# Optimization experiments

Hardware: AMD Instinct MI355X
Metric: run time of the kernel (lower is better)

The kernel has to match this reference:

```python
import jax, jax.numpy as jnp
import numpy as np

B, N, D, H, E = 4, 1024, 1024, 2048, 8

def setup_inputs() -> dict:
    key = jax.random.key(0)
    ks = jax.random.split(key, 5)
    return {
        "x": jax.random.normal(ks[0], (B, N, D), dtype=jnp.float32),
        "gate_w": jax.random.normal(ks[1], (D, E), dtype=jnp.float32) * 0.02,
        "gate_b": jnp.zeros((E,), dtype=jnp.float32),
        "w1": jax.random.normal(ks[2], (E, D, H), dtype=jnp.float32) * 0.02,
        "b1": jnp.zeros((E, H), dtype=jnp.float32),
        "w2": jax.random.normal(ks[3], (E, H, D), dtype=jnp.float32) * 0.02,
        "b2": jnp.zeros((E, D), dtype=jnp.float32),
        "gamma": jnp.ones((D,), dtype=jnp.float32),
    }

def reference(x, gate_w, gate_b, w1, b1, w2, b2, gamma):
    b, n, d = x.shape
    e = w1.shape[0]
    xf = x.reshape(b * n, d)                                    # [T, D]
    # gate: softmax over experts, then top-1
    probs = jax.nn.softmax(xf @ gate_w + gate_b, axis=-1)       # [T, E]
    top_val = jnp.max(probs, axis=-1, keepdims=True)            # [T, 1]
    top_idx = jnp.argmax(probs, axis=-1)                        # [T]
    # all-expert FFN (dense reference for masked dispatch; dropout in eval)
    h = jax.nn.gelu(jnp.einsum('td,edh->eth', xf, w1) + b1[:, None, :],
                    approximate=False)                          # [E, T, H]
    eo = jnp.einsum('eth,ehd->etd', h, w2) + b2[:, None, :]     # [E, T, D]
    onehot = jax.nn.one_hot(top_idx, e, dtype=xf.dtype)         # [T, E]
    out = jnp.einsum('etd,te->td', eo, onehot)                  # select routed expert
    y = (xf + out * top_val).reshape(b, n, d)
    # RMSNorm: F.normalize (L2, eps=1e-12) * gamma * sqrt(dim)
    nrm = jnp.linalg.norm(y, axis=-1, keepdims=True)
    y = y / jnp.maximum(nrm, 1e-12) * gamma * np.float32(np.sqrt(d))
    # load-balancing loss (unbiased variance like torch.var)
    importance = probs.sum(axis=0)                              # [E]
    load_loss = jnp.var(importance, ddof=1) / (jnp.mean(importance) ** 2 + 1e-10)
    return jax.nn.gelu(y, approximate=False), load_loss
```

## Files before the change

kernel.cpp:

```cpp
#include <hip/hip_runtime.h>
#include <math.h>

#define T_TOK 4096
#define DIM   1024
#define HID   2048
#define NE    8
#define TMM   128
#define BK    64
#define GATE_BLOCKS (T_TOK / 4)

typedef unsigned int  u32;
typedef unsigned short u16;
typedef __attribute__((ext_vector_type(8))) short bf16x8;
typedef __attribute__((ext_vector_type(4))) float f32x4;

__device__ __forceinline__ float gelu_exact(float v) {
    return 0.5f * v * (1.0f + erff(v * 0.70710678118654752440f));
}

__device__ __forceinline__ float gelu_fast(float x) {
    float u = 1.5957691216057308f * (x + 0.044715f * x * x * x);
    float e = __expf(u);
    float t = 1.f - 2.f / (e + 1.f);
    return 0.5f * x * (1.f + t);
}

__device__ __forceinline__ u16 f2bf(float v) {
    u32 u = __float_as_uint(v);
    u32 r = (u + 0x7FFFu + ((u >> 16) & 1u)) >> 16;
    return (u16)r;
}

__device__ __forceinline__ void gld_lds16(const void* g, void* l) {
    __builtin_amdgcn_global_load_lds(
        (const __attribute__((address_space(1))) u32*)g,
        (__attribute__((address_space(3))) u32*)l,
        16, 0, 0);
}

__device__ __forceinline__ void transpose_body(
    const float* __restrict__ in, u16* __restrict__ out, int R, int C,
    int bx, int by, int bz, float (*tile)[65])
{
    const float* src = in  + (size_t)bz * R * C;
    u16*         dst = out + (size_t)bz * R * C;
    const int c0 = bx * 64, r0 = by * 64;
    const int th = threadIdx.x;

    const int tr  = th >> 4;
    const int tc4 = (th & 15) * 4;
    #pragma unroll
    for (int i = 0; i < 4; i++) {
        const int r = tr + i * 16;
        float4 v = *(const float4*)&src[(size_t)(r0 + r) * C + c0 + tc4];
        tile[r][tc4 + 0] = v.x; tile[r][tc4 + 1] = v.y;
        tile[r][tc4 + 2] = v.z; tile[r][tc4 + 3] = v.w;
    }
    __syncthreads();
    const int cc  = th >> 4;
    const int rr4 = (th & 15) * 4;
    #pragma unroll
    for (int i = 0; i < 4; i++) {
        const int c = cc + i * 16;
        ushort4 o;
        o.x = f2bf(tile[rr4 + 0][c]);
        o.y = f2bf(tile[rr4 + 1][c]);
        o.z = f2bf(tile[rr4 + 2][c]);
        o.w = f2bf(tile[rr4 + 3][c]);
        *(ushort4*)&dst[(size_t)(c0 + c) * R + r0 + rr4] = o;
    }
}

__global__ __launch_bounds__(256) void prep_kernel(
    const float* __restrict__ w1, const float* __restrict__ w2,
    u16* __restrict__ w1t, u16* __restrict__ w2t,
    const float* __restrict__ x, const float* __restrict__ gw,
    const float* __restrict__ gb, float* __restrict__ top_val,
    int* __restrict__ top_idx, float* __restrict__ partial_imp,
    int* __restrict__ partial_cnt)
{
    __shared__ float tile[64][65];
    __shared__ float s_imp[NE];
    __shared__ int   s_cnt[NE];

    const int id = blockIdx.x;
    if (id < 4096) {
        transpose_body(w1, w1t, DIM, HID, id & 31, (id >> 5) & 15, id >> 9, tile);
        return;
    }
    if (id < 8192) {
        const int i2 = id - 4096;
        transpose_body(w2, w2t, HID, DIM, i2 & 15, (i2 >> 4) & 31, i2 >> 9, tile);
        return;
    }

    const int g = id - 8192;
    if (threadIdx.x < NE) { s_imp[threadIdx.x] = 0.f; s_cnt[threadIdx.x] = 0; }
    __syncthreads();

    const int wave = threadIdx.x >> 6;
    const int lane = threadIdx.x & 63;
    const int t = g * 4 + wave;

    float acc[NE];
    #pragma unroll
    for (int e = 0; e < NE; e++) acc[e] = 0.f;

    const float* xr = x + (size_t)t * DIM;
    #pragma unroll 4
    for (int k = lane; k < DIM; k += 64) {
        float xv = xr[k];
        const float* gp = gw + (size_t)k * NE;
        float4 g0 = *(const float4*)gp;
        float4 g1 = *(const float4*)(gp + 4);
        acc[0] += xv * g0.x; acc[1] += xv * g0.y;
        acc[2] += xv * g0.z; acc[3] += xv * g0.w;
        acc[4] += xv * g1.x; acc[5] += xv * g1.y;
        acc[6] += xv * g1.z; acc[7] += xv * g1.w;
    }
    #pragma unroll
    for (int e = 0; e < NE; e++) {
        #pragma unroll
        for (int off = 32; off > 0; off >>= 1)
            acc[e] += __shfl_down(acc[e], off, 64);
    }
    if (lane == 0) {
        float l[NE];
        float m = -1e30f;
        #pragma unroll
        for (int e = 0; e < NE; e++) { l[e] = acc[e] + gb[e]; m = fmaxf(m, l[e]); }
        float s = 0.f;
        #pragma unroll
        for (int e = 0; e < NE; e++) { l[e] = expf(l[e] - m); s += l[e]; }
        float inv = 1.f / s;
        int bi = 0; float bv = -1.f;
        #pragma unroll
        for (int e = 0; e < NE; e++) {
            float p = l[e] * inv;
            atomicAdd(&s_imp[e], p);
            if (p > bv) { bv = p; bi = e; }
        }
        top_val[t] = bv;
        top_idx[t] = bi;
        atomicAdd(&s_cnt[bi], 1);
    }
    __syncthreads();
    if (threadIdx.x < NE) {
        partial_imp[g * NE + threadIdx.x] = s_imp[threadIdx.x];
        partial_cnt[g * NE + threadIdx.x] = s_cnt[threadIdx.x];
    }
}

__global__ __launch_bounds__(256) void plan_kernel(
    const float* __restrict__ partial_imp, const int* __restrict__ partial_cnt,
    int* __restrict__ counts, int* __restrict__ offsets,
    int* __restrict__ tile_e, int* __restrict__ tile_s,
    int* __restrict__ tile_rows, int* __restrict__ ntiles,
    float* __restrict__ loss_out)
{
    __shared__ float rimp[32][NE];
    __shared__ int   rcnt[32][NE];
    const int th = threadIdx.x;
    const int e = th & 7, chunk = th >> 3;
    float si = 0.f; int sc = 0;
    #pragma unroll 8
    for (int i = 0; i < GATE_BLOCKS / 32; i++) {
        const int b = chunk * (GATE_BLOCKS / 32) + i;
        si += partial_imp[b * NE + e];
        sc += partial_cnt[b * NE + e];
    }
    rimp[chunk][e] = si;
    rcnt[chunk][e] = sc;
    __syncthreads();
    if (th < NE) {
        float s = 0.f; int c = 0;
        for (int i = 0; i < 32; i++) { s += rimp[i][th]; c += rcnt[i][th]; }
        counts[th] = c;
        rimp[0][th] = s;
        rcnt[0][th] = c;
    }
    __syncthreads();
    if (th == 0) {
        int off = 0, nt = 0;
        for (int ee = 0; ee < NE; ee++) {
            offsets[ee] = off;
            const int c = rcnt[0][ee];
            for (int s = 0; s < c; s += TMM) {
                tile_e[nt] = ee;
                tile_s[nt] = off + s;
                tile_rows[nt] = min(TMM, c - s);
                nt++;
            }
            off += c;
        }
        offsets[NE] = off;
        *ntiles = nt;

        float mean = 0.f;
        for (int ee = 0; ee < NE; ee++) mean += rimp[0][ee];
        mean *= (1.0f / NE);
        float var = 0.f;
        for (int ee = 0; ee < NE; ee++) { float d = rimp[0][ee] - mean; var += d * d; }
        var *= (1.0f / (NE - 1));
        loss_out[0] = var / (mean * mean + 1e-10f);
    }
}

__global__ __launch_bounds__(256) void scatter_kernel(
    const int* __restrict__ top_idx, const int* __restrict__ offsets,
    int* __restrict__ cursors, int* __restrict__ sorted_tok)
{
    __shared__ int lcnt[NE], lbase[NE];
    if (threadIdx.x < NE) lcnt[threadIdx.x] = 0;
    __syncthreads();
    const int t = blockIdx.x * blockDim.x + threadIdx.x;
    const int e = top_idx[t];
    const int lrank = atomicAdd(&lcnt[e], 1);
    __syncthreads();
    if (threadIdx.x < NE)
        lbase[threadIdx.x] = atomicAdd(&cursors[threadIdx.x], lcnt[threadIdx.x]);
    __syncthreads();
    sorted_tok[offsets[e] + lbase[e] + lrank] = t;
}

__global__ __launch_bounds__(256) void gather_x_kernel(
    const float* __restrict__ x, const int* __restrict__ sorted_tok,
    u16* __restrict__ xs)
{
    const int s = blockIdx.x;
    const int tok = sorted_tok[s];
    const float* src = x + (size_t)tok * DIM;
    u16* dst = xs + (size_t)s * DIM;
    const int i = threadIdx.x * 4;
    float4 v = *(const float4*)&src[i];
    ushort4 o;
    o.x = f2bf(v.x); o.y = f2bf(v.y); o.z = f2bf(v.z); o.w = f2bf(v.w);
    *(ushort4*)&dst[i] = o;
}

__global__ __launch_bounds__(512, 4) void ffn1_mfma(
    const u16* __restrict__ xs, const u16* __restrict__ w1t,
    const float* __restrict__ b1,
    const int* __restrict__ tile_e, const int* __restrict__ tile_s,
    const int* __restrict__ tile_rows, const int* __restrict__ ntiles,
    u16* __restrict__ h_buf)
{
    const int tile = blockIdx.y;
    if (tile >= *ntiles) return;
    const int e     = tile_e[tile];
    const int sbase = tile_s[tile];
    const int rows  = tile_rows[tile];
    const int nbase = blockIdx.x * 256;

    __shared__ __align__(16) u16 As[128 * BK];
    __shared__ __align__(16) u16 Bs[256 * BK];

    const int th = threadIdx.x;
    const int w  = th >> 6;
    const int l  = th & 63;
    const int wm = w >> 2, wn = w & 3;
    const int lr = l >> 3;
    const int lcs = ((l & 7) ^ lr) * 8;

    const u16* aptr[2];
    #pragma unroll
    for (int c = 0; c < 2; c++) {
        int srow = sbase + c * 64 + w * 8 + lr;
        if (srow > T_TOK - 1) srow = T_TOK - 1;
        aptr[c] = xs + (size_t)srow * DIM + lcs;
    }
    const u16* wb = w1t + (size_t)e * HID * DIM + (size_t)nbase * DIM;
    const u16* bptr[4];
    #pragma unroll
    for (int c = 0; c < 4; c++)
        bptr[c] = wb + (size_t)(c * 64 + w * 8 + lr) * DIM + lcs;

    f32x4 acc[4][4] = {};

    for (int k0 = 0; k0 < DIM; k0 += BK) {
        __syncthreads();
        #pragma unroll
        for (int c = 0; c < 2; c++)
            gld_lds16(aptr[c] + k0, &As[(c * 64 + w * 8) * BK]);
        #pragma unroll
        for (int c = 0; c < 4; c++)
            gld_lds16(bptr[c] + k0, &Bs[(c * 64 + w * 8) * BK]);
        __syncthreads();
        #pragma unroll
        for (int ks = 0; ks < 2; ks++) {
            const int ko = ((ks * 4 + (l >> 4)) ^ (l & 7)) * 8;
            bf16x8 af[4], bfr[4];
            #pragma unroll
            for (int i = 0; i < 4; i++)
                af[i]  = *(const bf16x8*)&As[(wm * 64 + i * 16 + (l & 15)) * BK + ko];
            #pragma unroll
            for (int i = 0; i < 4; i++)
                bfr[i] = *(const bf16x8*)&Bs[(wn * 64 + i * 16 + (l & 15)) * BK + ko];
            #pragma unroll
            for (int mi = 0; mi < 4; mi++)
                #pragma unroll
                for (int ni = 0; ni < 4; ni++)
                    acc[mi][ni] = __builtin_amdgcn_mfma_f32_16x16x32_bf16(
                        af[mi], bfr[ni], acc[mi][ni], 0, 0, 0);
        }
    }

    const int col = l & 15, quad = l >> 4;
    #pragma unroll
    for (int ni = 0; ni < 4; ni++) {
        const int n = nbase + wn * 64 + ni * 16 + col;
        const float bias = b1[e * HID + n];
        #pragma unroll
        for (int mi = 0; mi < 4; mi++) {
            #pragma unroll
            for (int r = 0; r < 4; r++) {
                const int m = wm * 64 + mi * 16 + quad * 4 + r;
                if (m < rows) {
                    float v = acc[mi][ni][r] + bias;
                    h_buf[(size_t)(sbase + m) * HID + n] = f2bf(gelu_fast(v));
                }
            }
        }
    }
}

__global__ __launch_bounds__(256) void ffn2_mfma(
    const u16* __restrict__ h_buf, const u16* __restrict__ w2t,
    const float* __restrict__ b2, const float* __restrict__ x,
    const int* __restrict__ sorted_tok, const float* __restrict__ top_val,
    const int* __restrict__ tile_e, const int* __restrict__ tile_s,
    const int* __restrict__ tile_rows, const int* __restrict__ ntiles,
    float* __restrict__ yout)
{
    const int tile = blockIdx.y;
    if (tile >= *ntiles) return;
    const int e     = tile_e[tile];
    const int sbase = tile_s[tile];
    const int rows  = tile_rows[tile];
    const int nbase = blockIdx.x * 128;

    __shared__ __align__(16) u16 As[128 * BK];
    __shared__ __align__(16) u16 Bs[128 * BK];

    const int th = threadIdx.x;
    const int w  = th >> 6;
    const int l  = th & 63;
    const int wm = w >> 1, wn = w & 1;
    const int lr = l >> 3;
    const int lcs = ((l & 7) ^ lr) * 8;

    const u16* aptr[4];
    #pragma unroll
    for (int c = 0; c < 4; c++) {
        int srow = sbase + w * 32 + c * 8 + lr;
        if (srow > T_TOK - 1) srow = T_TOK - 1;
        aptr[c] = h_buf + (size_t)srow * HID + lcs;
    }
    const u16* wb = w2t + (size_t)e * DIM * HID + (size_t)nbase * HID;
    const u16* bptr[4];
    #pragma unroll
    for (int c = 0; c < 4; c++)
        bptr[c] = wb + (size_t)(w * 32 + c * 8 + lr) * HID + lcs;

    f32x4 acc[4][4] = {};

    for (int k0 = 0; k0 < HID; k0 += BK) {
        __syncthreads();
        #pragma unroll
        for (int c = 0; c < 4; c++)
            gld_lds16(aptr[c] + k0, &As[(w * 32 + c * 8) * BK]);
        #pragma unroll
        for (int c = 0; c < 4; c++)
            gld_lds16(bptr[c] + k0, &Bs[(w * 32 + c * 8) * BK]);
        __syncthreads();
        #pragma unroll
        for (int ks = 0; ks < 2; ks++) {
            const int ko = ((ks * 4 + (l >> 4)) ^ (l & 7)) * 8;
            bf16x8 af[4], bfr[4];
            #pragma unroll
            for (int i = 0; i < 4; i++)
                af[i]  = *(const bf16x8*)&As[(wm * 64 + i * 16 + (l & 15)) * BK + ko];
            #pragma unroll
            for (int i = 0; i < 4; i++)
                bfr[i] = *(const bf16x8*)&Bs[(wn * 64 + i * 16 + (l & 15)) * BK + ko];
            #pragma unroll
            for (int mi = 0; mi < 4; mi++)
                #pragma unroll
                for (int ni = 0; ni < 4; ni++)
                    acc[mi][ni] = __builtin_amdgcn_mfma_f32_16x16x32_bf16(
                        af[mi], bfr[ni], acc[mi][ni], 0, 0, 0);
        }
    }

    const int col = l & 15, quad = l >> 4;
    float bias[4];
    #pragma unroll
    for (int ni = 0; ni < 4; ni++)
        bias[ni] = b2[e * DIM + nbase + wn * 64 + ni * 16 + col];

    #pragma unroll
    for (int mi = 0; mi < 4; mi++) {
        #pragma unroll
        for (int r = 0; r < 4; r++) {
            const int m = wm * 64 + mi * 16 + quad * 4 + r;
            if (m < rows) {
                const int t = sorted_tok[sbase + m];
                const float tv = top_val[t];
                #pragma unroll
                for (int ni = 0; ni < 4; ni++) {
                    const int n = nbase + wn * 64 + ni * 16 + col;
                    float v = acc[mi][ni][r] + bias[ni];
                    yout[(size_t)t * DIM + n] = x[(size_t)t * DIM + n] + v * tv;
                }
            }
        }
    }
}

__global__ __launch_bounds__(256) void norm_kernel(float* __restrict__ y,
                                                   const float* __restrict__ gamma)
{
    const int t = blockIdx.x;
    float* row = y + (size_t)t * DIM;
    const int th = threadIdx.x;
    float4 v = *(const float4*)&row[th * 4];
    float ss = v.x * v.x + v.y * v.y + v.z * v.z + v.w * v.w;

    const int lane = th & 63, wave = th >> 6;
    #pragma unroll
    for (int off = 32; off > 0; off >>= 1) ss += __shfl_down(ss, off, 64);
    __shared__ float red[4];
    if (lane == 0) red[wave] = ss;
    __syncthreads();
    float total = red[0] + red[1] + red[2] + red[3];

    float nrm = sqrtf(total);
    float scale = 32.0f / fmaxf(nrm, 1e-12f);

    float4 g = *(const float4*)&gamma[th * 4];
    float4 o;
    o.x = gelu_exact(v.x * scale * g.x);
    o.y = gelu_exact(v.y * scale * g.y);
    o.z = gelu_exact(v.z * scale * g.z);
    o.w = gelu_exact(v.w * scale * g.w);
    *(float4*)&row[th * 4] = o;
}

extern "C" void kernel_launch(void* const* d_in, const int* in_sizes, int n_in,
                              void* d_out, int out_size, void* d_ws, size_t ws_size,
                              hipStream_t stream) {
    const float* x      = (const float*)d_in[0];
    const float* gate_w = (const float*)d_in[1];
    const float* gate_b = (const float*)d_in[2];
    const float* w1     = (const float*)d_in[3];
    const float* b1     = (const float*)d_in[4];
    const float* w2     = (const float*)d_in[5];
    const float* b2     = (const float*)d_in[6];
    const float* gamma  = (const float*)d_in[7];

    float* out  = (float*)d_out;
    float* loss = out + (size_t)T_TOK * DIM;

    char* ws = (char*)d_ws;
    float* top_val     = (float*)(ws + 0);
    int*   top_idx     = (int*)  (ws + 16384);
    int*   sorted_tok  = (int*)  (ws + 32768);
    int*   counts      = (int*)  (ws + 49152);
    int*   cursors     = (int*)  (ws + 49216);
    int*   offsets     = (int*)  (ws + 49280);
    int*   tile_e      = (int*)  (ws + 49664);
    int*   tile_s      = (int*)  (ws + 50176);
    int*   tile_rows   = (int*)  (ws + 50688);
    int*   ntiles      = (int*)  (ws + 51200);
    float* partial_imp = (float*)(ws + 65536);
    int*   partial_cnt = (int*)  (ws + 98304);
    u16*   x_sorted    = (u16*)  (ws + 131072);
    u16*   h_buf       = (u16*)  (ws + 131072 + 8388608);
    u16*   w1t         = (u16*)  (ws + 131072 + 8388608 + 16777216);
    u16*   w2t         = (u16*)  (ws + 131072 + 8388608 + 16777216 + 33554432);

    hipMemsetAsync(ws + 49216, 0, 64, stream);

    prep_kernel<<<8192 + GATE_BLOCKS, 256, 0, stream>>>(
        w1, w2, w1t, w2t, x, gate_w, gate_b, top_val, top_idx,
        partial_imp, partial_cnt);
    plan_kernel<<<1, 256, 0, stream>>>(partial_imp, partial_cnt, counts,
                                       offsets, tile_e, tile_s, tile_rows,
                                       ntiles, loss);
    scatter_kernel<<<T_TOK / 256, 256, 0, stream>>>(top_idx, offsets, cursors,
                                                    sorted_tok);
    gather_x_kernel<<<T_TOK, 256, 0, stream>>>(x, sorted_tok, x_sorted);

    ffn1_mfma<<<dim3(HID / 256, 40), 512, 0, stream>>>(
        x_sorted, w1t, b1, tile_e, tile_s, tile_rows, ntiles, h_buf);
    ffn2_mfma<<<dim3(DIM / 128, 40), 256, 0, stream>>>(
        h_buf, w2t, b2, x, sorted_tok, top_val, tile_e, tile_s, tile_rows,
        ntiles, out);
    norm_kernel<<<T_TOK, 256, 0, stream>>>(out, gamma);
}
```

Before: 300.3 us.

## Merge plan and scatter kernels, shrink FFN1 tiles, swap grid axes

Widens the transpose stores in the weight-prep kernel to 8-element bf16 vectors. Folds the scatter step into the single-block plan kernel, which removes one launch, the memset and the global atomics on cursors. Shrinks the FFN1 block tile from 128x256 with 512 threads to 128x128 with 256 threads. Swaps grid axes in both FFN kernels so token tiles vary fastest along blockIdx.x. The serial single-block scatter and the smaller FFN1 tiles, which reload the activation tile more often, may offset the gains.

```diff
diff --git a/kernel.cpp b/kernel.cpp
--- a/kernel.cpp
+++ b/kernel.cpp
@@ -12,6 +12,7 @@
 typedef unsigned int  u32;
 typedef unsigned short u16;
 typedef __attribute__((ext_vector_type(8))) short bf16x8;
+typedef __attribute__((ext_vector_type(8))) unsigned short u16x8;
 typedef __attribute__((ext_vector_type(4))) float f32x4;
 
 __device__ __forceinline__ float gelu_exact(float v) {
@@ -57,17 +58,15 @@
         tile[r][tc4 + 2] = v.z; tile[r][tc4 + 3] = v.w;
     }
     __syncthreads();
-    const int cc  = th >> 4;
-    const int rr4 = (th & 15) * 4;
-    #pragma unroll
-    for (int i = 0; i < 4; i++) {
-        const int c = cc + i * 16;
-        ushort4 o;
-        o.x = f2bf(tile[rr4 + 0][c]);
-        o.y = f2bf(tile[rr4 + 1][c]);
-        o.z = f2bf(tile[rr4 + 2][c]);
-        o.w = f2bf(tile[rr4 + 3][c]);
-        *(ushort4*)&dst[(size_t)(c0 + c) * R + r0 + rr4] = o;
+    const int cc  = th >> 3;
+    const int rr8 = (th & 7) * 8;
+    #pragma unroll
+    for (int i = 0; i < 2; i++) {
+        const int c = cc + i * 32;
+        u16x8 o;
+        #pragma unroll
+        for (int j = 0; j < 8; j++) o[j] = f2bf(tile[rr8 + j][c]);
+        *(u16x8*)&dst[(size_t)(c0 + c) * R + r0 + rr8] = o;
     }
 }
 
@@ -151,15 +150,18 @@
     }
 }
 
-__global__ __launch_bounds__(256) void plan_kernel(
+__global__ __launch_bounds__(256) void route_kernel(
     const float* __restrict__ partial_imp, const int* __restrict__ partial_cnt,
-    int* __restrict__ counts, int* __restrict__ offsets,
+    const int* __restrict__ top_idx,
+    int* __restrict__ sorted_tok,
     int* __restrict__ tile_e, int* __restrict__ tile_s,
     int* __restrict__ tile_rows, int* __restrict__ ntiles,
     float* __restrict__ loss_out)
 {
     __shared__ float rimp[32][NE];
     __shared__ int   rcnt[32][NE];
+    __shared__ int   s_off[NE];
+    __shared__ int   s_cur[NE];
     const int th = threadIdx.x;
     const int e = th & 7, chunk = th >> 3;
     float si = 0.f; int sc = 0;
@@ -175,15 +177,15 @@
     if (th < NE) {
         float s = 0.f; int c = 0;
         for (int i = 0; i < 32; i++) { s += rimp[i][th]; c += rcnt[i][th]; }
-        counts[th] = c;
         rimp[0][th] = s;
         rcnt[0][th] = c;
+        s_cur[th] = 0;
     }
     __syncthreads();
     if (th == 0) {
         int off = 0, nt = 0;
         for (int ee = 0; ee < NE; ee++) {
-            offsets[ee] = off;
+            s_off[ee] = off;
             const int c = rcnt[0][ee];
             for (int s = 0; s < c; s += TMM) {
                 tile_e[nt] = ee;
@@ -193,7 +195,6 @@
             }
             off += c;
         }
-        offsets[NE] = off;
         *ntiles = nt;
 
         float mean = 0.f;
@@ -204,23 +205,15 @@
         var *= (1.0f / (NE - 1));
         loss_out[0] = var / (mean * mean + 1e-10f);
     }
-}
-
-__global__ __launch_bounds__(256) void scatter_kernel(
-    const int* __restrict__ top_idx, const int* __restrict__ offsets,
-    int* __restrict__ cursors, int* __restrict__ sorted_tok)
-{
-    __shared__ int lcnt[NE], lbase[NE];
-    if (threadIdx.x < NE) lcnt[threadIdx.x] = 0;
-    __syncthreads();
-    const int t = blockIdx.x * blockDim.x + threadIdx.x;
-    const int e = top_idx[t];
-    const int lrank = atomicAdd(&lcnt[e], 1);
-    __syncthreads();
-    if (threadIdx.x < NE)
-        lbase[threadIdx.x] = atomicAdd(&cursors[threadIdx.x], lcnt[threadIdx.x]);
-    __syncthreads();
-    sorted_tok[offsets[e] + lbase[e] + lrank] = t;
+    __syncthreads();
+
+    #pragma unroll 4
+    for (int r = 0; r < T_TOK / 256; r++) {
+        const int t  = r * 256 + th;
+        const int te = top_idx[t];
+        const int rank = atomicAdd(&s_cur[te], 1);
+        sorted_tok[s_off[te] + rank] = t;
+    }
 }
 
 __global__ __launch_bounds__(256) void gather_x_kernel(
@@ -238,34 +231,34 @@
     *(ushort4*)&dst[i] = o;
 }
 
-__global__ __launch_bounds__(512, 4) void ffn1_mfma(
+__global__ __launch_bounds__(256) void ffn1_mfma(
     const u16* __restrict__ xs, const u16* __restrict__ w1t,
     const float* __restrict__ b1,
     const int* __restrict__ tile_e, const int* __restrict__ tile_s,
     const int* __restrict__ tile_rows, const int* __restrict__ ntiles,
     u16* __restrict__ h_buf)
 {
-    const int tile = blockIdx.y;
+    const int tile = blockIdx.x;
     if (tile >= *ntiles) return;
     const int e     = tile_e[tile];
     const int sbase = tile_s[tile];
     const int rows  = tile_rows[tile];
-    const int nbase = blockIdx.x * 256;
+    const int nbase = blockIdx.y * 128;
 
     __shared__ __align__(16) u16 As[128 * BK];
-    __shared__ __align__(16) u16 Bs[256 * BK];
+    __shared__ __align__(16) u16 Bs[128 * BK];
 
     const int th = threadIdx.x;
     const int w  = th >> 6;
     const int l  = th & 63;
-    const int wm = w >> 2, wn = w & 3;
+    const int wm = w >> 1, wn = w & 1;
     const int lr = l >> 3;
     const int lcs = ((l & 7) ^ lr) * 8;
 
-    const u16* aptr[2];
-    #pragma unroll
-    for (int c = 0; c < 2; c++) {
-        int srow = sbase + c * 64 + w * 8 + lr;
+    const u16* aptr[4];
+    #pragma unroll
+    for (int c = 0; c < 4; c++) {
+        int srow = sbase + w * 32 + c * 8 + lr;
         if (srow > T_TOK - 1) srow = T_TOK - 1;
         aptr[c] = xs + (size_t)srow * DIM + lcs;
     }
@@ -273,18 +266,18 @@
     const u16* bptr[4];
     #pragma unroll
     for (int c = 0; c < 4; c++)
-        bptr[c] = wb + (size_t)(c * 64 + w * 8 + lr) * DIM + lcs;
+        bptr[c] = wb + (size_t)(w * 32 + c * 8 + lr) * DIM + lcs;
 
     f32x4 acc[4][4] = {};
 
     for (int k0 = 0; k0 < DIM; k0 += BK) {
         __syncthreads();
         #pragma unroll
-        for (int c = 0; c < 2; c++)
-            gld_lds16(aptr[c] + k0, &As[(c * 64 + w * 8) * BK]);
-        #pragma unroll
         for (int c = 0; c < 4; c++)
-            gld_lds16(bptr[c] + k0, &Bs[(c * 64 + w * 8) * BK]);
+            gld_lds16(aptr[c] + k0, &As[(w * 32 + c * 8) * BK]);
+        #pragma unroll
+        for (int c = 0; c < 4; c++)
+            gld_lds16(bptr[c] + k0, &Bs[(w * 32 + c * 8) * BK]);
         __syncthreads();
         #pragma unroll
         for (int ks = 0; ks < 2; ks++) {
@@ -332,12 +325,12 @@
     const int* __restrict__ tile_rows, const int* __restrict__ ntiles,
     float* __restrict__ yout)
 {
-    const int tile = blockIdx.y;
+    const int tile = blockIdx.x;
     if (tile >= *ntiles) return;
     const int e     = tile_e[tile];
     const int sbase = tile_s[tile];
     const int rows  = tile_rows[tile];
-    const int nbase = blockIdx.x * 128;
+    const int nbase = blockIdx.y * 128;
 
     __shared__ __align__(16) u16 As[128 * BK];
     __shared__ __align__(16) u16 Bs[128 * BK];
@@ -465,9 +458,6 @@
     float* top_val     = (float*)(ws + 0);
     int*   top_idx     = (int*)  (ws + 16384);
     int*   sorted_tok  = (int*)  (ws + 32768);
-    int*   counts      = (int*)  (ws + 49152);
-    int*   cursors     = (int*)  (ws + 49216);
-    int*   offsets     = (int*)  (ws + 49280);
     int*   tile_e      = (int*)  (ws + 49664);
     int*   tile_s      = (int*)  (ws + 50176);
     int*   tile_rows   = (int*)  (ws + 50688);
@@ -479,21 +469,17 @@
     u16*   w1t         = (u16*)  (ws + 131072 + 8388608 + 16777216);
     u16*   w2t         = (u16*)  (ws + 131072 + 8388608 + 16777216 + 33554432);
 
-    hipMemsetAsync(ws + 49216, 0, 64, stream);
-
     prep_kernel<<<8192 + GATE_BLOCKS, 256, 0, stream>>>(
         w1, w2, w1t, w2t, x, gate_w, gate_b, top_val, top_idx,
         partial_imp, partial_cnt);
-    plan_kernel<<<1, 256, 0, stream>>>(partial_imp, partial_cnt, counts,
-                                       offsets, tile_e, tile_s, tile_rows,
-                                       ntiles, loss);
-    scatter_kernel<<<T_TOK / 256, 256, 0, stream>>>(top_idx, offsets, cursors,
-                                                    sorted_tok);
+    route_kernel<<<1, 256, 0, stream>>>(partial_imp, partial_cnt, top_idx,
+                                        sorted_tok, tile_e, tile_s, tile_rows,
+                                        ntiles, loss);
     gather_x_kernel<<<T_TOK, 256, 0, stream>>>(x, sorted_tok, x_sorted);
 
-    ffn1_mfma<<<dim3(HID / 256, 40), 512, 0, stream>>>(
+    ffn1_mfma<<<dim3(40, HID / 128), 256, 0, stream>>>(
         x_sorted, w1t, b1, tile_e, tile_s, tile_rows, ntiles, h_buf);
-    ffn2_mfma<<<dim3(DIM / 128, 40), 256, 0, stream>>>(
+    ffn2_mfma<<<dim3(40, DIM / 128), 256, 0, stream>>>(
         h_buf, w2t, b2, x, sorted_tok, top_val, tile_e, tile_s, tile_rows,
         ntiles, out);
     norm_kernel<<<T_TOK, 256, 0, stream>>>(out, gamma);
```

Result: slower. 315.3 us (+5.0%).
